# Optimization experiments

Hardware: AMD Instinct MI355X
Metric: run time of the kernel (lower is better)

The kernel has to match this reference:

```python
import jax, jax.numpy as jnp
import numpy as np

B, S, D, H, C = 64, 512, 768, 768, 5


def setup_inputs() -> dict:
    key = jax.random.key(0)
    ks = jax.random.split(key, 7)
    return {
        "hidden_states": jax.random.normal(ks[0], (B, S, D), jnp.float32),
        "mask": jnp.ones((B, S), dtype=bool),
        # Dense(hidden_size, relu)
        "W1": jax.random.normal(ks[1], (D, H), jnp.float32) * 0.02,
        "b1": jnp.zeros((H,), jnp.float32),
        # CRF inner dense -> potentials over num_classes
        "W2": jax.random.normal(ks[2], (H, C), jnp.float32) * 0.02,
        "b2": jnp.zeros((C,), jnp.float32),
        # CRF transition matrix and boundary energies (tfa use_boundary=True)
        "chain_kernel": jax.random.normal(ks[3], (C, C), jnp.float32) * 0.1,
        "left_boundary": jax.random.normal(ks[4], (C,), jnp.float32) * 0.1,
        "right_boundary": jax.random.normal(ks[5], (C,), jnp.float32) * 0.1,
    }


def viterbi_decode(potentials, trans):
    """potentials: [B,S,C], trans: [C,C] -> decoded tags [B,S] int32."""
    pot_t = jnp.swapaxes(potentials, 0, 1)  # [S,B,C]

    def fwd_step(alpha, pot):
        scores = alpha[:, :, None] + trans[None]      # [B,C_prev,C_cur]
        bp = jnp.argmax(scores, axis=1)               # [B,C]
        alpha = jnp.max(scores, axis=1) + pot         # [B,C]
        return alpha, bp

    alpha, bps = jax.lax.scan(fwd_step, pot_t[0], pot_t[1:])  # bps: [S-1,B,C]
    last = jnp.argmax(alpha, axis=-1).astype(jnp.int32)       # [B]

    def back_step(tag, bp):
        prev = jnp.take_along_axis(bp, tag[:, None], axis=1)[:, 0].astype(jnp.int32)
        return prev, prev

    _, tags = jax.lax.scan(back_step, last, bps, reverse=True)  # [S-1,B]
    decoded = jnp.concatenate([jnp.swapaxes(tags, 0, 1), last[:, None]], axis=1)
    return decoded


def reference(hidden_states, mask, W1, b1, W2, b2, chain_kernel,
              left_boundary, right_boundary):
    # Dense + ReLU (dropout is identity at inference / training=False)
    h = jax.nn.relu(jnp.einsum('bsd,dh->bsh', hidden_states, W1) + b1)
    # CRF inner dense -> unary potentials
    pot = jnp.einsum('bsh,hc->bsc', h, W2) + b2
    # boundary energies at first / last timestep (mask is full-length here)
    pot = pot.at[:, 0].add(left_boundary).at[:, -1].add(right_boundary)
    seq_length = jnp.sum(mask.astype(jnp.int32), axis=1)
    decoded = viterbi_decode(pot, chain_kernel)
    return decoded, pot, seq_length, chain_kernel
```

## Files before the change

kernel.cpp:

```cpp
#include <hip/hip_runtime.h>

#define B_  64
#define S_  512
#define D_  768
#define H_  768
#define C_  5
#define M_  (B_ * S_)

typedef float f32x4 __attribute__((ext_vector_type(4)));
typedef short short8 __attribute__((ext_vector_type(8)));

#define W1T_ELEMS (D_ * H_)
#define XBF_ELEMS (M_ * D_)

__device__ __forceinline__ unsigned short f2bf(float f) {
    unsigned int u = __float_as_uint(f);
    u += 0x7FFFu + ((u >> 16) & 1u);
    return (unsigned short)(u >> 16);
}

__global__ __launch_bounds__(256) void init_pot_kernel(
    const float* __restrict__ b2, const float* __restrict__ lb,
    const float* __restrict__ rb, float* __restrict__ pot)
{
    const int idx = blockIdx.x * 256 + threadIdx.x;
    if (idx < M_ * C_) {
        const int c = idx % C_;
        const int t = (idx / C_) & (S_ - 1);
        float v = b2[c];
        if (t == 0)      v += lb[c];
        if (t == S_ - 1) v += rb[c];
        pot[idx] = v;
    }
}

__global__ __launch_bounds__(256) void prep_w1_kernel(
    const float* __restrict__ W1, unsigned short* __restrict__ w1t)
{
    __shared__ float t[32][33];
    const int bx = blockIdx.x;
    const int by = blockIdx.y;
    const int lx = threadIdx.x & 31, ly = threadIdx.x >> 5;
    #pragma unroll
    for (int j = 0; j < 4; ++j)
        t[ly + 8 * j][lx] = W1[(by * 32 + ly + 8 * j) * H_ + bx * 32 + lx];
    __syncthreads();
    #pragma unroll
    for (int j = 0; j < 4; ++j)
        w1t[(size_t)(bx * 32 + ly + 8 * j) * D_ + by * 32 + lx] = f2bf(t[lx][ly + 8 * j]);
}

__global__ __launch_bounds__(256) void prep_x_kernel(
    const float* __restrict__ X, unsigned short* __restrict__ xbf)
{
    const size_t i0 = ((size_t)blockIdx.x * 256 + threadIdx.x) * 8;
    const float4 a = *(const float4*)(X + i0);
    const float4 b = *(const float4*)(X + i0 + 4);
    union { unsigned short u[8]; uint4 v; } o;
    o.u[0] = f2bf(a.x); o.u[1] = f2bf(a.y); o.u[2] = f2bf(a.z); o.u[3] = f2bf(a.w);
    o.u[4] = f2bf(b.x); o.u[5] = f2bf(b.y); o.u[6] = f2bf(b.z); o.u[7] = f2bf(b.w);
    *(uint4*)(xbf + i0) = o.v;
}

__device__ __forceinline__ void gload16(const void* g, void* l) {
    __builtin_amdgcn_global_load_lds(
        (const __attribute__((address_space(1))) unsigned int*)g,
        (__attribute__((address_space(3))) unsigned int*)l, 16, 0, 0);
}

__global__ __launch_bounds__(256) void gemm_bf16x2_kernel(
    const unsigned short* __restrict__ xbf,
    const unsigned short* __restrict__ w1t,
    const float* __restrict__ b1,
    const float* __restrict__ W2,
    float* __restrict__ pot)
{
    __shared__ __align__(16) unsigned short Asm[2][128 * 32];
    __shared__ __align__(16) unsigned short Bsm[2][128 * 32];
    __shared__ float pp[2][128][C_];

    const int tid  = threadIdx.x;
    const int lane = tid & 63, w = tid >> 6;
    const int wm   = w >> 1, wn = w & 1;
    const int i15  = lane & 15, quad = lane >> 4;

    const int bid = blockIdx.x;
    const int r8 = bid & 7, q8 = bid >> 3;
    const int nb = q8 % 6, mhi = q8 / 6;
    const int m0 = (mhi * 8 + r8) * 128;
    const int n0 = nb * 128;

    const unsigned short* gA[2];
    const unsigned short* gB[2];
    int lofsA[2], lofsB[2];
    #pragma unroll
    for (int i = 0; i < 2; ++i) {
        const int g = 2 * w + i;
        gA[i] = xbf + (size_t)(m0 + g * 16 + i15) * D_ + quad * 8;
        gB[i] = w1t + (size_t)(n0 + g * 16 + i15) * D_ + quad * 8;
        lofsA[i] = g * 512;
        lofsB[i] = g * 512;
    }

    f32x4 acc[4][4];
    #pragma unroll
    for (int mi = 0; mi < 4; ++mi)
        #pragma unroll
        for (int ni = 0; ni < 4; ++ni)
            acc[mi][ni] = (f32x4){0.f, 0.f, 0.f, 0.f};

    #pragma unroll
    for (int i = 0; i < 2; ++i) {
        gload16(gA[i], &Asm[0][lofsA[i]]); gA[i] += 32;
        gload16(gB[i], &Bsm[0][lofsB[i]]); gB[i] += 32;
    }
    __syncthreads();

    #define KITERS (D_ / 32)
    for (int kt = 0; kt < KITERS; ++kt) {
        const int cur = kt & 1, nxt = cur ^ 1;

        if (kt + 1 < KITERS) {
            #pragma unroll
            for (int i = 0; i < 2; ++i) {
                gload16(gA[i], &Asm[nxt][lofsA[i]]); gA[i] += 32;
                gload16(gB[i], &Bsm[nxt][lofsB[i]]); gB[i] += 32;
            }
        }

        short8 af[4], bfr[4];
        #pragma unroll
        for (int mi = 0; mi < 4; ++mi)
            af[mi] = *(const short8*)&Asm[cur][(wm * 4 + mi) * 512 + quad * 128 + i15 * 8];
        #pragma unroll
        for (int ni = 0; ni < 4; ++ni)
            bfr[ni] = *(const short8*)&Bsm[cur][(wn * 4 + ni) * 512 + quad * 128 + i15 * 8];

        #pragma unroll
        for (int ni = 0; ni < 4; ++ni)
            #pragma unroll
            for (int mi = 0; mi < 4; ++mi)
                acc[mi][ni] = __builtin_amdgcn_mfma_f32_16x16x32_bf16(
                    af[mi], bfr[ni], acc[mi][ni], 0, 0, 0);

        __syncthreads();
    }

    float b1v[4], w2v[4][C_];
    #pragma unroll
    for (int ni = 0; ni < 4; ++ni) {
        const int col = n0 + wn * 64 + ni * 16 + i15;
        b1v[ni] = b1[col];
        #pragma unroll
        for (int cc = 0; cc < C_; ++cc) w2v[ni][cc] = W2[col * C_ + cc];
    }

    #pragma unroll
    for (int mi = 0; mi < 4; ++mi) {
        float ps[4][C_];
        #pragma unroll
        for (int r = 0; r < 4; ++r)
            #pragma unroll
            for (int cc = 0; cc < C_; ++cc) ps[r][cc] = 0.f;

        #pragma unroll
        for (int ni = 0; ni < 4; ++ni)
            #pragma unroll
            for (int r = 0; r < 4; ++r) {
                float h = acc[mi][ni][r] + b1v[ni];
                h = h > 0.f ? h : 0.f;
                #pragma unroll
                for (int cc = 0; cc < C_; ++cc)
                    ps[r][cc] = fmaf(h, w2v[ni][cc], ps[r][cc]);
            }

        #pragma unroll
        for (int off = 1; off < 16; off <<= 1)
            #pragma unroll
            for (int r = 0; r < 4; ++r)
                #pragma unroll
                for (int cc = 0; cc < C_; ++cc)
                    ps[r][cc] += __shfl_xor(ps[r][cc], off, 64);

        if (i15 == 0) {
            #pragma unroll
            for (int r = 0; r < 4; ++r) {
                const int row = wm * 64 + mi * 16 + quad * 4 + r;
                #pragma unroll
                for (int cc = 0; cc < C_; ++cc)
                    pp[wn][row][cc] = ps[r][cc];
            }
        }
    }
    __syncthreads();

    for (int idx = tid; idx < 128 * C_; idx += 256) {
        const int row = idx / C_, cc = idx % C_;
        atomicAdd(&pot[(size_t)(m0 + row) * C_ + cc],
                  pp[0][row][cc] + pp[1][row][cc]);
    }
}

__global__ __launch_bounds__(256) void gemm_bf16_kernel(
    const float* __restrict__ X,
    const unsigned short* __restrict__ w1t,
    const float* __restrict__ b1,
    const float* __restrict__ W2,
    float* __restrict__ pot)
{
    __shared__ __align__(16) float          Asm[128 * 32];
    __shared__ __align__(16) unsigned short Bsm[128 * 32];
    __shared__ float pp[2][128][C_];

    const int tid  = threadIdx.x;
    const int lane = tid & 63, w = tid >> 6;
    const int wm   = w >> 1, wn = w & 1;
    const int i15  = lane & 15, quad = lane >> 4;

    const int bid = blockIdx.x;
    const int r8 = bid & 7, q8 = bid >> 3;
    const int nb = q8 % 6, mhi = q8 / 6;
    const int m0 = (mhi * 8 + r8) * 128;
    const int n0 = nb * 128;

    const float* gA[4];
    float* lA[4];
    const unsigned short* gB[2];
    unsigned short* lB[2];
    #pragma unroll
    for (int i = 0; i < 4; ++i) {
        const int a = 4 * w + i, g = a >> 1, h = a & 1;
        gA[i] = X + (size_t)(m0 + g * 16 + i15) * D_ + (4 * h + quad) * 4;
        lA[i] = &Asm[g * 512 + h * 256];
    }
    #pragma unroll
    for (int i = 0; i < 2; ++i) {
        const int b = 2 * w + i;
        gB[i] = w1t + (size_t)(n0 + b * 16 + i15) * D_ + quad * 8;
        lB[i] = &Bsm[b * 512];
    }

    f32x4 acc[4][4];
    #pragma unroll
    for (int mi = 0; mi < 4; ++mi)
        #pragma unroll
        for (int ni = 0; ni < 4; ++ni)
            acc[mi][ni] = (f32x4){0.f, 0.f, 0.f, 0.f};

    for (int kt = 0; kt < D_ / 32; ++kt) {
        __syncthreads();
        #pragma unroll
        for (int i = 0; i < 4; ++i) { gload16(gA[i], lA[i]); gA[i] += 32; }
        #pragma unroll
        for (int i = 0; i < 2; ++i) { gload16(gB[i], lB[i]); gB[i] += 32; }
        __syncthreads();

        short8 af[4];
        #pragma unroll
        for (int mi = 0; mi < 4; ++mi) {
            const int row = wm * 64 + mi * 16 + i15;
            const int base = (row >> 4) * 512 + (row & 15) * 4 + quad * 128;
            const f32x4 lo = *(const f32x4*)&Asm[base];
            const f32x4 hi = *(const f32x4*)&Asm[base + 64];
            float f[8];
            *(f32x4*)&f[0] = lo; *(f32x4*)&f[4] = hi;
            union { short8 s; unsigned short u[8]; } cv;
            #pragma unroll
            for (int j = 0; j < 8; ++j) cv.u[j] = f2bf(f[j]);
            af[mi] = cv.s;
        }
        short8 bfr[4];
        #pragma unroll
        for (int ni = 0; ni < 4; ++ni) {
            const int row = wn * 64 + ni * 16 + i15;
            bfr[ni] = *(const short8*)&Bsm[(row >> 4) * 512 + quad * 128 + (row & 15) * 8];
        }
        #pragma unroll
        for (int ni = 0; ni < 4; ++ni)
            #pragma unroll
            for (int mi = 0; mi < 4; ++mi)
                acc[mi][ni] = __builtin_amdgcn_mfma_f32_16x16x32_bf16(
                    af[mi], bfr[ni], acc[mi][ni], 0, 0, 0);
    }

    float b1v[4], w2v[4][C_];
    #pragma unroll
    for (int ni = 0; ni < 4; ++ni) {
        const int col = n0 + wn * 64 + ni * 16 + i15;
        b1v[ni] = b1[col];
        #pragma unroll
        for (int cc = 0; cc < C_; ++cc) w2v[ni][cc] = W2[col * C_ + cc];
    }

    #pragma unroll
    for (int mi = 0; mi < 4; ++mi) {
        float ps[4][C_];
        #pragma unroll
        for (int r = 0; r < 4; ++r)
            #pragma unroll
            for (int cc = 0; cc < C_; ++cc) ps[r][cc] = 0.f;

        #pragma unroll
        for (int ni = 0; ni < 4; ++ni)
            #pragma unroll
            for (int r = 0; r < 4; ++r) {
                float h = acc[mi][ni][r] + b1v[ni];
                h = h > 0.f ? h : 0.f;
                #pragma unroll
                for (int cc = 0; cc < C_; ++cc)
                    ps[r][cc] = fmaf(h, w2v[ni][cc], ps[r][cc]);
            }

        #pragma unroll
        for (int off = 1; off < 16; off <<= 1)
            #pragma unroll
            for (int r = 0; r < 4; ++r)
                #pragma unroll
                for (int cc = 0; cc < C_; ++cc)
                    ps[r][cc] += __shfl_xor(ps[r][cc], off, 64);

        if (i15 == 0) {
            #pragma unroll
            for (int r = 0; r < 4; ++r) {
                const int row = wm * 64 + mi * 16 + quad * 4 + r;
                #pragma unroll
                for (int cc = 0; cc < C_; ++cc)
                    pp[wn][row][cc] = ps[r][cc];
            }
        }
    }
    __syncthreads();

    for (int idx = tid; idx < 128 * C_; idx += 256) {
        const int row = idx / C_, cc = idx % C_;
        atomicAdd(&pot[(size_t)(m0 + row) * C_ + cc],
                  pp[0][row][cc] + pp[1][row][cc]);
    }
}

#define FBK 8
#define FLDS 132
__global__ __launch_bounds__(256) void gemm_relu_pot_kernel(
    const float* __restrict__ X, const float* __restrict__ W1,
    const float* __restrict__ b1, const float* __restrict__ W2,
    float* __restrict__ pot)
{
    __shared__ float As[FBK * FLDS];
    __shared__ float Bs[FBK * FLDS];
    __shared__ float w2s[128][C_];

    const int tid = threadIdx.x;
    const int tx = tid & 15, ty = tid >> 4;
    const int m0 = blockIdx.y * 128, n0 = blockIdx.x * 128;

    for (int idx = tid; idx < 128 * C_; idx += 256)
        w2s[idx / C_][idx % C_] = W2[(n0 + idx / C_) * C_ + idx % C_];

    float acc[2][2][4][4];
    #pragma unroll
    for (int a = 0; a < 2; ++a)
        #pragma unroll
        for (int b = 0; b < 2; ++b)
            #pragma unroll
            for (int i = 0; i < 4; ++i)
                #pragma unroll
                for (int j = 0; j < 4; ++j) acc[a][b][i][j] = 0.f;

    const int arow = tid >> 1, aq = tid & 1;
    const int brow = tid >> 5, bq = tid & 31;
    const float* Aptr = X + (m0 + arow) * D_ + aq * 4;
    const float* Bptr = W1 + brow * H_ + n0 + bq * 4;

    for (int kt = 0; kt < D_; kt += FBK) {
        const float4 avv = *(const float4*)Aptr;
        const float4 bvv = *(const float4*)Bptr;
        __syncthreads();
        As[(aq * 4 + 0) * FLDS + arow] = avv.x;
        As[(aq * 4 + 1) * FLDS + arow] = avv.y;
        As[(aq * 4 + 2) * FLDS + arow] = avv.z;
        As[(aq * 4 + 3) * FLDS + arow] = avv.w;
        *(float4*)&Bs[brow * FLDS + bq * 4] = bvv;
        __syncthreads();
        #pragma unroll
        for (int k = 0; k < FBK; ++k) {
            const float4 a0 = *(const float4*)&As[k * FLDS + (ty << 2)];
            const float4 a1 = *(const float4*)&As[k * FLDS + 64 + (ty << 2)];
            const float4 b0 = *(const float4*)&Bs[k * FLDS + (tx << 2)];
            const float4 b1r = *(const float4*)&Bs[k * FLDS + 64 + (tx << 2)];
            const float ar[2][4] = {{a0.x,a0.y,a0.z,a0.w},{a1.x,a1.y,a1.z,a1.w}};
            const float br[2][4] = {{b0.x,b0.y,b0.z,b0.w},{b1r.x,b1r.y,b1r.z,b1r.w}};
            #pragma unroll
            for (int ri = 0; ri < 2; ++ri)
                #pragma unroll
                for (int i = 0; i < 4; ++i)
                    #pragma unroll
                    for (int rj = 0; rj < 2; ++rj)
                        #pragma unroll
                        for (int j = 0; j < 4; ++j)
                            acc[ri][rj][i][j] = fmaf(ar[ri][i], br[rj][j], acc[ri][rj][i][j]);
        }
        Aptr += FBK;
        Bptr += FBK * H_;
    }

    float ps[2][4][C_];
    #pragma unroll
    for (int ri = 0; ri < 2; ++ri)
        #pragma unroll
        for (int i = 0; i < 4; ++i)
            #pragma unroll
            for (int cc = 0; cc < C_; ++cc) ps[ri][i][cc] = 0.f;

    #pragma unroll
    for (int rj = 0; rj < 2; ++rj)
        #pragma unroll
        for (int j = 0; j < 4; ++j) {
            const int nl = rj * 64 + (tx << 2) + j;
            const float bj = b1[n0 + nl];
            float w2c[C_];
            #pragma unroll
            for (int cc = 0; cc < C_; ++cc) w2c[cc] = w2s[nl][cc];
            #pragma unroll
            for (int ri = 0; ri < 2; ++ri)
                #pragma unroll
                for (int i = 0; i < 4; ++i) {
                    float h = acc[ri][rj][i][j] + bj;
                    h = h > 0.f ? h : 0.f;
                    #pragma unroll
                    for (int cc = 0; cc < C_; ++cc)
                        ps[ri][i][cc] = fmaf(h, w2c[cc], ps[ri][i][cc]);
                }
        }

    #pragma unroll
    for (int off = 1; off < 16; off <<= 1)
        #pragma unroll
        for (int ri = 0; ri < 2; ++ri)
            #pragma unroll
            for (int i = 0; i < 4; ++i)
                #pragma unroll
                for (int cc = 0; cc < C_; ++cc)
                    ps[ri][i][cc] += __shfl_xor(ps[ri][i][cc], off, 64);

    if (tx == 0)
        #pragma unroll
        for (int ri = 0; ri < 2; ++ri)
            #pragma unroll
            for (int i = 0; i < 4; ++i) {
                const int m = m0 + ri * 64 + (ty << 2) + i;
                #pragma unroll
                for (int cc = 0; cc < C_; ++cc)
                    atomicAdd(&pot[m * C_ + cc], ps[ri][i][cc]);
            }
}

__global__ __launch_bounds__(64) void viterbi_kernel(
    const float* __restrict__ pot, const float* __restrict__ trans,
    const int* __restrict__ mask, float* __restrict__ decoded,
    float* __restrict__ seqlen, float* __restrict__ chain_out)
{
    const int b = blockIdx.x;
    const int lane = threadIdx.x;

    __shared__ float pl[S_ * C_];
    __shared__ unsigned int bpk[S_];
    __shared__ unsigned int gseg[64];
    __shared__ int bt[64];
    __shared__ int dec_s[S_];
    __shared__ int s_last;

    const float* pb = pot + b * (S_ * C_);
    for (int i = lane; i < S_ * C_; i += 64) pl[i] = pb[i];

    int mcnt = 0;
    const int* mb = mask + b * S_;
    for (int i = lane; i < S_; i += 64) mcnt += (mb[i] != 0) ? 1 : 0;
    #pragma unroll
    for (int off = 32; off >= 1; off >>= 1) mcnt += __shfl_xor(mcnt, off, 64);

    if (b == 0 && lane < C_ * C_) chain_out[lane] = trans[lane];

    float tr[C_][C_];
    #pragma unroll
    for (int p = 0; p < C_; ++p)
        #pragma unroll
        for (int c = 0; c < C_; ++c) tr[p][c] = trans[p * C_ + c];

    __syncthreads();

    const float NEG = -1.0e30f;

    float G[C_][C_];
    #pragma unroll
    for (int c = 0; c < C_; ++c)
        #pragma unroll
        for (int p = 0; p < C_; ++p) G[c][p] = (c == p) ? 0.f : NEG;

    for (int j = 1; j <= 8; ++j) {
        const int t = 8 * lane + j;
        if (t < S_) {
            float ng[C_][C_];
            #pragma unroll
            for (int c = 0; c < C_; ++c) {
                const float pc = pl[t * C_ + c];
                #pragma unroll
                for (int p = 0; p < C_; ++p) {
                    float m = tr[0][c] + G[0][p];
                    #pragma unroll
                    for (int q = 1; q < C_; ++q)
                        m = fmaxf(m, tr[q][c] + G[q][p]);
                    ng[c][p] = m + pc;
                }
            }
            #pragma unroll
            for (int c = 0; c < C_; ++c)
                #pragma unroll
                for (int p = 0; p < C_; ++p) G[c][p] = ng[c][p];
        }
    }

    #pragma unroll
    for (int d = 1; d < 64; d <<= 1) {
        float Q[C_][C_];
        #pragma unroll
        for (int q = 0; q < C_; ++q)
            #pragma unroll
            for (int p = 0; p < C_; ++p) Q[q][p] = __shfl_up(G[q][p], d, 64);
        if (lane >= d) {
            float ng[C_][C_];
            #pragma unroll
            for (int c = 0; c < C_; ++c)
                #pragma unroll
                for (int p = 0; p < C_; ++p) {
                    float m = G[c][0] + Q[0][p];
                    #pragma unroll
                    for (int q = 1; q < C_; ++q)
                        m = fmaxf(m, G[c][q] + Q[q][p]);
                    ng[c][p] = m;
                }
            #pragma unroll
            for (int c = 0; c < C_; ++c)
                #pragma unroll
                for (int p = 0; p < C_; ++p) G[c][p] = ng[c][p];
        }
    }

    float a[C_];
    {
        float E[C_][C_];
        #pragma unroll
        for (int c = 0; c < C_; ++c)
            #pragma unroll
            for (int p = 0; p < C_; ++p) E[c][p] = __shfl_up(G[c][p], 1, 64);
        float a0[C_];
        #pragma unroll
        for (int c = 0; c < C_; ++c) a0[c] = pl[c];
        if (lane == 0) {
            #pragma unroll
            for (int c = 0; c < C_; ++c) a[c] = a0[c];
        } else {
            #pragma unroll
            for (int c = 0; c < C_; ++c) {
                float m = E[c][0] + a0[0];
                #pragma unroll
                for (int q = 1; q < C_; ++q) m = fmaxf(m, E[c][q] + a0[q]);
                a[c] = m;
            }
        }
    }

    for (int j = 1; j <= 8; ++j) {
        const int t = 8 * lane + j;
        if (t < S_) {
            unsigned int mpack = 0;
            float na[C_];
            #pragma unroll
            for (int c = 0; c < C_; ++c) {
                float best = a[0] + tr[0][c];
                int arg = 0;
                #pragma unroll
                for (int p = 1; p < C_; ++p) {
                    const float s = a[p] + tr[p][c];
                    if (s > best) { best = s; arg = p; }
                }
                mpack |= (unsigned int)arg << (3 * c);
                na[c] = best + pl[t * C_ + c];
            }
            bpk[t] = mpack;
            #pragma unroll
            for (int c = 0; c < C_; ++c) a[c] = na[c];
        }
    }

    if (lane == 63) {
        float best = a[0];
        int arg = 0;
        #pragma unroll
        for (int p = 1; p < C_; ++p)
            if (a[p] > best) { best = a[p]; arg = p; }
        s_last = arg;
    }
    if (lane == 0) bpk[0] = 0;
    __syncthreads();

    const int last = s_last;

    unsigned int g = 0u | (1u << 3) | (2u << 6) | (3u << 9) | (4u << 12);
    #pragma unroll
    for (int j = 7; j >= 0; --j) {
        const int t = 8 * lane + j;
        if (t >= 1) {
            const unsigned int m = bpk[t];
            unsigned int ng = 0;
            #pragma unroll
            for (int x = 0; x < C_; ++x) {
                const unsigned int gx = (g >> (3 * x)) & 7u;
                ng |= ((m >> (3 * gx)) & 7u) << (3 * x);
            }
            g = ng;
        }
    }
    gseg[lane] = g;
    __syncthreads();

    if (lane == 0) {
        int cur = last;
        for (int l = 63; l >= 0; --l) {
            bt[l] = cur;
            cur = (int)((gseg[l] >> (3 * cur)) & 7u);
        }
        seqlen[b] = (float)mcnt;
    }
    __syncthreads();

    {
        int tag = bt[lane];
        const int t0 = 8 * lane;
        dec_s[t0 + 7] = tag;
        #pragma unroll
        for (int t = t0 + 7; t >= t0 + 1; --t) {
            tag = (int)((bpk[t] >> (3 * tag)) & 7u);
            dec_s[t - 1] = tag;
        }
    }
    __syncthreads();

    float* db = decoded + b * S_;
    for (int i = lane; i < S_; i += 64) db[i] = (float)dec_s[i];
}

extern "C" void kernel_launch(void* const* d_in, const int* in_sizes, int n_in,
                              void* d_out, int out_size, void* d_ws, size_t ws_size,
                              hipStream_t stream) {
    const float* hs    = (const float*)d_in[0];
    const int*   mask  = (const int*)  d_in[1];
    const float* W1    = (const float*)d_in[2];
    const float* b1    = (const float*)d_in[3];
    const float* W2    = (const float*)d_in[4];
    const float* b2    = (const float*)d_in[5];
    const float* chain = (const float*)d_in[6];
    const float* lb    = (const float*)d_in[7];
    const float* rb    = (const float*)d_in[8];

    float* out      = (float*)d_out;
    float* decoded  = out;
    float* pot      = out + M_;
    float* seq      = out + M_ + M_ * C_;
    float* chainout = seq + B_;

    init_pot_kernel<<<(M_ * C_ + 255) / 256, 256, 0, stream>>>(b2, lb, rb, pot);

    const size_t need_w1 = (size_t)W1T_ELEMS * sizeof(unsigned short);
    const size_t need_all = need_w1 + (size_t)XBF_ELEMS * sizeof(unsigned short);

    if (ws_size >= need_all) {
        unsigned short* w1t = (unsigned short*)d_ws;
        unsigned short* xbf = w1t + W1T_ELEMS;
        dim3 pgrid(H_ / 32, D_ / 32);
        prep_w1_kernel<<<pgrid, 256, 0, stream>>>(W1, w1t);
        prep_x_kernel<<<XBF_ELEMS / (256 * 8), 256, 0, stream>>>(hs, xbf);
        gemm_bf16x2_kernel<<<1536, 256, 0, stream>>>(xbf, w1t, b1, W2, pot);
    } else if (ws_size >= need_w1) {
        unsigned short* w1t = (unsigned short*)d_ws;
        dim3 pgrid(H_ / 32, D_ / 32);
        prep_w1_kernel<<<pgrid, 256, 0, stream>>>(W1, w1t);
        gemm_bf16_kernel<<<1536, 256, 0, stream>>>(hs, w1t, b1, W2, pot);
    } else {
        dim3 grid(H_ / 128, M_ / 128);
        gemm_relu_pot_kernel<<<grid, 256, 0, stream>>>(hs, W1, b1, W2, pot);
    }

    viterbi_kernel<<<B_, 64, 0, stream>>>(pot, chain, mask, decoded, seq, chainout);
}
```

Before: 285.9 us.

## Fuse prep kernels into one launch and double GEMM K-tile to 64

Merges the X bf16 conversion, W1 transpose/convert and potential initialisation into a single kernel launch, which removes two launch overheads and lets the three jobs overlap. The GEMM now stages 64-wide K tiles (two 32-wide chunks) per double-buffer step, halving the number of barriers and main-loop iterations. The epilogue's partial-sum scratch now reuses the A shared buffer instead of a separate array. The larger tiles double LDS use per block, which may lower occupancy.

```diff
diff --git a/kernel.cpp b/kernel.cpp
--- a/kernel.cpp
+++ b/kernel.cpp
@@ -13,10 +13,73 @@
 #define W1T_ELEMS (D_ * H_)
 #define XBF_ELEMS (M_ * D_)
 
+#define PX_BLOCKS   (XBF_ELEMS / (256 * 8))
+#define PW_BLOCKS   ((D_ / 32) * (H_ / 32))
+#define PI_BLOCKS   ((M_ * C_ + 255) / 256)
+
 __device__ __forceinline__ unsigned short f2bf(float f) {
     unsigned int u = __float_as_uint(f);
     u += 0x7FFFu + ((u >> 16) & 1u);
     return (unsigned short)(u >> 16);
+}
+
+__global__ __launch_bounds__(256) void prep_all_kernel(
+    const float* __restrict__ X, const float* __restrict__ W1,
+    const float* __restrict__ b2, const float* __restrict__ lb,
+    const float* __restrict__ rb,
+    unsigned short* __restrict__ xbf, unsigned short* __restrict__ w1t,
+    float* __restrict__ pot)
+{
+    __shared__ float t[32][33];
+    const int bid = blockIdx.x;
+    const int tid = threadIdx.x;
+
+    if (bid < PX_BLOCKS) {
+        const size_t i0 = ((size_t)bid * 256 + tid) * 8;
+        const float4 a = *(const float4*)(X + i0);
+        const float4 b = *(const float4*)(X + i0 + 4);
+        union { unsigned short u[8]; uint4 v; } o;
+        o.u[0] = f2bf(a.x); o.u[1] = f2bf(a.y); o.u[2] = f2bf(a.z); o.u[3] = f2bf(a.w);
+        o.u[4] = f2bf(b.x); o.u[5] = f2bf(b.y); o.u[6] = f2bf(b.z); o.u[7] = f2bf(b.w);
+        *(uint4*)(xbf + i0) = o.v;
+    } else if (bid < PX_BLOCKS + PW_BLOCKS) {
+        const int b2i = bid - PX_BLOCKS;
+        const int bx = b2i % (H_ / 32);
+        const int by = b2i / (H_ / 32);
+        const int lx = tid & 31, ly = tid >> 5;
+        #pragma unroll
+        for (int j = 0; j < 4; ++j)
+            t[ly + 8 * j][lx] = W1[(by * 32 + ly + 8 * j) * H_ + bx * 32 + lx];
+        __syncthreads();
+        #pragma unroll
+        for (int j = 0; j < 4; ++j)
+            w1t[(size_t)(bx * 32 + ly + 8 * j) * D_ + by * 32 + lx] = f2bf(t[lx][ly + 8 * j]);
+    } else {
+        const int idx = (bid - PX_BLOCKS - PW_BLOCKS) * 256 + tid;
+        if (idx < M_ * C_) {
+            const int c = idx % C_;
+            const int tt = (idx / C_) & (S_ - 1);
+            float v = b2[c];
+            if (tt == 0)      v += lb[c];
+            if (tt == S_ - 1) v += rb[c];
+            pot[idx] = v;
+        }
+    }
+}
+
+__global__ __launch_bounds__(256) void prep_w1_kernel(
+    const float* __restrict__ W1, unsigned short* __restrict__ w1t)
+{
+    __shared__ float t[32][33];
+    const int bx = blockIdx.x, by = blockIdx.y;
+    const int lx = threadIdx.x & 31, ly = threadIdx.x >> 5;
+    #pragma unroll
+    for (int j = 0; j < 4; ++j)
+        t[ly + 8 * j][lx] = W1[(by * 32 + ly + 8 * j) * H_ + bx * 32 + lx];
+    __syncthreads();
+    #pragma unroll
+    for (int j = 0; j < 4; ++j)
+        w1t[(size_t)(bx * 32 + ly + 8 * j) * D_ + by * 32 + lx] = f2bf(t[lx][ly + 8 * j]);
 }
 
 __global__ __launch_bounds__(256) void init_pot_kernel(
@@ -34,50 +97,21 @@
     }
 }
 
-__global__ __launch_bounds__(256) void prep_w1_kernel(
-    const float* __restrict__ W1, unsigned short* __restrict__ w1t)
-{
-    __shared__ float t[32][33];
-    const int bx = blockIdx.x;
-    const int by = blockIdx.y;
-    const int lx = threadIdx.x & 31, ly = threadIdx.x >> 5;
-    #pragma unroll
-    for (int j = 0; j < 4; ++j)
-        t[ly + 8 * j][lx] = W1[(by * 32 + ly + 8 * j) * H_ + bx * 32 + lx];
-    __syncthreads();
-    #pragma unroll
-    for (int j = 0; j < 4; ++j)
-        w1t[(size_t)(bx * 32 + ly + 8 * j) * D_ + by * 32 + lx] = f2bf(t[lx][ly + 8 * j]);
-}
-
-__global__ __launch_bounds__(256) void prep_x_kernel(
-    const float* __restrict__ X, unsigned short* __restrict__ xbf)
-{
-    const size_t i0 = ((size_t)blockIdx.x * 256 + threadIdx.x) * 8;
-    const float4 a = *(const float4*)(X + i0);
-    const float4 b = *(const float4*)(X + i0 + 4);
-    union { unsigned short u[8]; uint4 v; } o;
-    o.u[0] = f2bf(a.x); o.u[1] = f2bf(a.y); o.u[2] = f2bf(a.z); o.u[3] = f2bf(a.w);
-    o.u[4] = f2bf(b.x); o.u[5] = f2bf(b.y); o.u[6] = f2bf(b.z); o.u[7] = f2bf(b.w);
-    *(uint4*)(xbf + i0) = o.v;
-}
-
 __device__ __forceinline__ void gload16(const void* g, void* l) {
     __builtin_amdgcn_global_load_lds(
         (const __attribute__((address_space(1))) unsigned int*)g,
         (__attribute__((address_space(3))) unsigned int*)l, 16, 0, 0);
 }
 
-__global__ __launch_bounds__(256) void gemm_bf16x2_kernel(
+__global__ __launch_bounds__(256) void gemm_bk64_kernel(
     const unsigned short* __restrict__ xbf,
     const unsigned short* __restrict__ w1t,
     const float* __restrict__ b1,
     const float* __restrict__ W2,
     float* __restrict__ pot)
 {
-    __shared__ __align__(16) unsigned short Asm[2][128 * 32];
-    __shared__ __align__(16) unsigned short Bsm[2][128 * 32];
-    __shared__ float pp[2][128][C_];
+    __shared__ __align__(16) unsigned short Asm[2][8192];
+    __shared__ __align__(16) unsigned short Bsm[2][8192];
 
     const int tid  = threadIdx.x;
     const int lane = tid & 63, w = tid >> 6;
@@ -92,14 +126,13 @@
 
     const unsigned short* gA[2];
     const unsigned short* gB[2];
-    int lofsA[2], lofsB[2];
+    int lofs[2];
     #pragma unroll
     for (int i = 0; i < 2; ++i) {
         const int g = 2 * w + i;
         gA[i] = xbf + (size_t)(m0 + g * 16 + i15) * D_ + quad * 8;
         gB[i] = w1t + (size_t)(n0 + g * 16 + i15) * D_ + quad * 8;
-        lofsA[i] = g * 512;
-        lofsB[i] = g * 512;
+        lofs[i] = g * 512;
     }
 
     f32x4 acc[4][4];
@@ -111,40 +144,51 @@
 
     #pragma unroll
     for (int i = 0; i < 2; ++i) {
-        gload16(gA[i], &Asm[0][lofsA[i]]); gA[i] += 32;
-        gload16(gB[i], &Bsm[0][lofsB[i]]); gB[i] += 32;
-    }
-    __syncthreads();
-
-    #define KITERS (D_ / 32)
+        gload16(gA[i],      &Asm[0][lofs[i]]);
+        gload16(gA[i] + 32, &Asm[0][4096 + lofs[i]]);
+        gload16(gB[i],      &Bsm[0][lofs[i]]);
+        gload16(gB[i] + 32, &Bsm[0][4096 + lofs[i]]);
+        gA[i] += 64; gB[i] += 64;
+    }
+    __syncthreads();
+
+    #define KITERS (D_ / 64)
     for (int kt = 0; kt < KITERS; ++kt) {
         const int cur = kt & 1, nxt = cur ^ 1;
 
         if (kt + 1 < KITERS) {
             #pragma unroll
             for (int i = 0; i < 2; ++i) {
-                gload16(gA[i], &Asm[nxt][lofsA[i]]); gA[i] += 32;
-                gload16(gB[i], &Bsm[nxt][lofsB[i]]); gB[i] += 32;
-            }
-        }
-
-        short8 af[4], bfr[4];
-        #pragma unroll
-        for (int mi = 0; mi < 4; ++mi)
-            af[mi] = *(const short8*)&Asm[cur][(wm * 4 + mi) * 512 + quad * 128 + i15 * 8];
-        #pragma unroll
-        for (int ni = 0; ni < 4; ++ni)
-            bfr[ni] = *(const short8*)&Bsm[cur][(wn * 4 + ni) * 512 + quad * 128 + i15 * 8];
-
-        #pragma unroll
-        for (int ni = 0; ni < 4; ++ni)
+                gload16(gA[i],      &Asm[nxt][lofs[i]]);
+                gload16(gA[i] + 32, &Asm[nxt][4096 + lofs[i]]);
+                gload16(gB[i],      &Bsm[nxt][lofs[i]]);
+                gload16(gB[i] + 32, &Bsm[nxt][4096 + lofs[i]]);
+                gA[i] += 64; gB[i] += 64;
+            }
+        }
+
+        #pragma unroll
+        for (int c = 0; c < 2; ++c) {
+            const int cb = c * 4096;
+            short8 af[4], bfr[4];
             #pragma unroll
             for (int mi = 0; mi < 4; ++mi)
-                acc[mi][ni] = __builtin_amdgcn_mfma_f32_16x16x32_bf16(
-                    af[mi], bfr[ni], acc[mi][ni], 0, 0, 0);
+                af[mi] = *(const short8*)&Asm[cur][cb + (wm * 4 + mi) * 512 + quad * 128 + i15 * 8];
+            #pragma unroll
+            for (int ni = 0; ni < 4; ++ni)
+                bfr[ni] = *(const short8*)&Bsm[cur][cb + (wn * 4 + ni) * 512 + quad * 128 + i15 * 8];
+            #pragma unroll
+            for (int ni = 0; ni < 4; ++ni)
+                #pragma unroll
+                for (int mi = 0; mi < 4; ++mi)
+                    acc[mi][ni] = __builtin_amdgcn_mfma_f32_16x16x32_bf16(
+                        af[mi], bfr[ni], acc[mi][ni], 0, 0, 0);
+        }
 
         __syncthreads();
     }
+
+    float* pp = (float*)&Asm[0][0];
 
     float b1v[4], w2v[4][C_];
     #pragma unroll
@@ -188,7 +232,7 @@
                 const int row = wm * 64 + mi * 16 + quad * 4 + r;
                 #pragma unroll
                 for (int cc = 0; cc < C_; ++cc)
-                    pp[wn][row][cc] = ps[r][cc];
+                    pp[(wn * 128 + row) * C_ + cc] = ps[r][cc];
             }
         }
     }
@@ -197,7 +241,7 @@
     for (int idx = tid; idx < 128 * C_; idx += 256) {
         const int row = idx / C_, cc = idx % C_;
         atomicAdd(&pot[(size_t)(m0 + row) * C_ + cc],
-                  pp[0][row][cc] + pp[1][row][cc]);
+                  pp[row * C_ + cc] + pp[(128 + row) * C_ + cc]);
     }
 }
 
@@ -668,24 +712,23 @@
     float* seq      = out + M_ + M_ * C_;
     float* chainout = seq + B_;
 
-    init_pot_kernel<<<(M_ * C_ + 255) / 256, 256, 0, stream>>>(b2, lb, rb, pot);
-
     const size_t need_w1 = (size_t)W1T_ELEMS * sizeof(unsigned short);
     const size_t need_all = need_w1 + (size_t)XBF_ELEMS * sizeof(unsigned short);
 
     if (ws_size >= need_all) {
         unsigned short* w1t = (unsigned short*)d_ws;
         unsigned short* xbf = w1t + W1T_ELEMS;
-        dim3 pgrid(H_ / 32, D_ / 32);
-        prep_w1_kernel<<<pgrid, 256, 0, stream>>>(W1, w1t);
-        prep_x_kernel<<<XBF_ELEMS / (256 * 8), 256, 0, stream>>>(hs, xbf);
-        gemm_bf16x2_kernel<<<1536, 256, 0, stream>>>(xbf, w1t, b1, W2, pot);
+        prep_all_kernel<<<PX_BLOCKS + PW_BLOCKS + PI_BLOCKS, 256, 0, stream>>>(
+            hs, W1, b2, lb, rb, xbf, w1t, pot);
+        gemm_bk64_kernel<<<1536, 256, 0, stream>>>(xbf, w1t, b1, W2, pot);
     } else if (ws_size >= need_w1) {
         unsigned short* w1t = (unsigned short*)d_ws;
+        init_pot_kernel<<<PI_BLOCKS, 256, 0, stream>>>(b2, lb, rb, pot);
         dim3 pgrid(H_ / 32, D_ / 32);
         prep_w1_kernel<<<pgrid, 256, 0, stream>>>(W1, w1t);
         gemm_bf16_kernel<<<1536, 256, 0, stream>>>(hs, w1t, b1, W2, pot);
     } else {
+        init_pot_kernel<<<PI_BLOCKS, 256, 0, stream>>>(b2, lb, rb, pot);
         dim3 grid(H_ / 128, M_ / 128);
         gemm_relu_pot_kernel<<<grid, 256, 0, stream>>>(hs, W1, b1, W2, pot);
     }
```

Result: faster. 272.9 us (-4.6%).
